# Performance work log

Hardware: AMD Instinct MI355X
Metric: run time of the kernel (lower is better)

Reference implementation:

```python
import jax, jax.numpy as jnp
import numpy as np

NEG_BIG = -9e15
ALPHA = 0.2  # leakyrelu slope


def setup_inputs() -> dict:
    key = jax.random.key(0)
    k1, k2, k3, k4 = jax.random.split(key, 4)
    N, Fin, Fout = 8192, 256, 256
    input = jax.random.normal(k1, (N, Fin), dtype=jnp.float32)
    adj = jax.random.randint(k2, (N, N), 0, 2, dtype=jnp.int32)
    W = jax.random.normal(k3, (Fin, Fout), dtype=jnp.float32) * (1.0 / np.sqrt(Fin))
    a = jax.random.normal(k4, (2 * Fout, 1), dtype=jnp.float32) * (1.0 / np.sqrt(Fout))
    return {"input": input, "adj": adj, "W": W, "a": a}


def reference(input, adj, W, a):
    # h: [N, F]
    h = input @ W
    Fout = h.shape[1]
    # Fused score: e_ij = leakyrelu(h_i . a[:F] + h_j . a[F:])
    s1 = h @ a[:Fout, 0]   # [N]
    s2 = h @ a[Fout:, 0]   # [N]
    e = s1[:, None] + s2[None, :]            # [N, N]
    e = jnp.where(e >= 0, e, ALPHA * e)      # leaky relu
    e = jnp.where(adj > 0, e, NEG_BIG)       # mask
    attention = jax.nn.softmax(e, axis=1)    # row softmax
    h_prime = attention @ h                  # [N, F]
    return jax.nn.elu(h_prime)               # concat=True -> elu
```

## Files before the change

kernel.cpp:

```cpp
#include <hip/hip_runtime.h>
#include <hip/hip_bf16.h>

#define LRALPHA 0.2f
#define LOG2E 1.4426950408889634f

typedef __attribute__((ext_vector_type(8))) short frag_ab;
typedef __attribute__((ext_vector_type(4))) float frag_cd;
typedef int   iv4 __attribute__((ext_vector_type(4)));
typedef float fv4 __attribute__((ext_vector_type(4)));
typedef unsigned int uv4 __attribute__((ext_vector_type(4)));
typedef unsigned int uv2 __attribute__((ext_vector_type(2)));

static __device__ __forceinline__ unsigned short f2bf(float f) {
  __hip_bfloat16 b = __float2bfloat16(f);
  unsigned short u;
  __builtin_memcpy(&u, &b, 2);
  return u;
}

#if __has_builtin(__builtin_amdgcn_exp2f)
#define EXP2F(x) __builtin_amdgcn_exp2f(x)
#else
#define EXP2F(x) exp2f(x)
#endif

static __device__ __forceinline__ unsigned cvt_pk_bf16(float lo, float hi) {
  unsigned r;
  asm("v_cvt_pk_bf16_f32 %0, %1, %2" : "=v"(r) : "v"(lo), "v"(hi));
  return r;
}

static __device__ __forceinline__ void block_sync_lds() {
  __builtin_amdgcn_sched_barrier(0);
  asm volatile("s_waitcnt lgkmcnt(0)" ::: "memory");
  __builtin_amdgcn_s_barrier();
  __builtin_amdgcn_sched_barrier(0);
}

static __device__ __forceinline__ uv2 make_w4(iv4 ca, fv4 cv,
                                              float s1r, float mr, float& zloc) {
  float w[4];
#pragma unroll
  for (int e = 0; e < 4; ++e) {
    float ee = s1r + cv[e];
    ee = fmaxf(ee, LRALPHA * ee);
    float ww = EXP2F(ee - mr);
    ww = ca[e] ? ww : 0.f;
    zloc += ww;
    w[e] = ww;
  }
  uv2 r;
  r[0] = cvt_pk_bf16(w[0], w[1]);
  r[1] = cvt_pk_bf16(w[2], w[3]);
  return r;
}

__global__ __launch_bounds__(256, 4) void gat_hproj(
    const float* __restrict__ X, const float* __restrict__ W,
    const float* __restrict__ avec,
    float* __restrict__ s1, float* __restrict__ s2,
    unsigned short* __restrict__ hT) {
  const int tid = threadIdx.x;
  const int row0 = blockIdx.x * 16;
  const float* Xb = X + (size_t)row0 * 256;
  const int c = tid;

  float acc[16];
#pragma unroll
  for (int r = 0; r < 16; ++r) acc[r] = 0.f;

  for (int k = 0; k < 256; k += 4) {
    const float w0 = W[(k + 0) * 256 + c];
    const float w1 = W[(k + 1) * 256 + c];
    const float w2 = W[(k + 2) * 256 + c];
    const float w3 = W[(k + 3) * 256 + c];
#pragma unroll
    for (int r = 0; r < 16; ++r) {
      acc[r] = fmaf(Xb[r * 256 + k + 0], w0, acc[r]);
      acc[r] = fmaf(Xb[r * 256 + k + 1], w1, acc[r]);
      acc[r] = fmaf(Xb[r * 256 + k + 2], w2, acc[r]);
      acc[r] = fmaf(Xb[r * 256 + k + 3], w3, acc[r]);
    }
  }

  alignas(16) unsigned short hu[16];
#pragma unroll
  for (int r = 0; r < 16; ++r) hu[r] = f2bf(acc[r]);
  uv4* hdst = (uv4*)(hT + (size_t)c * 8192 + row0);
  hdst[0] = *(const uv4*)&hu[0];
  hdst[1] = *(const uv4*)&hu[8];

  const float a1c = avec[c];
  const float a2c = avec[256 + c];
  const int lane = tid & 63, wave = tid >> 6;
  __shared__ float r1[4][16], r2[4][16];
#pragma unroll
  for (int r = 0; r < 16; ++r) {
    float v1 = acc[r] * a1c;
    float v2 = acc[r] * a2c;
#pragma unroll
    for (int off = 32; off > 0; off >>= 1) {
      v1 += __shfl_down(v1, off);
      v2 += __shfl_down(v2, off);
    }
    if (lane == 0) { r1[wave][r] = v1; r2[wave][r] = v2; }
  }
  __syncthreads();
  if (tid < 16) {
    s1[row0 + tid] = (r1[0][tid] + r1[1][tid] + r1[2][tid] + r1[3][tid]) * LOG2E;
    s2[row0 + tid] = (r2[0][tid] + r2[1][tid] + r2[2][tid] + r2[3][tid]) * LOG2E;
  }
}

__global__ __launch_bounds__(512, 2) void gat_attn_full(
    const int* __restrict__ adj, const unsigned short* __restrict__ hT,
    const float* __restrict__ s1, const float* __restrict__ s2,
    float* __restrict__ out) {
  const int bid = blockIdx.x;
  const int row0 = bid * 32;
  const int tid = threadIdx.x;
  const int wave = tid >> 6, lane = tid & 63;
  const int ln16 = lane & 15, quad = lane >> 4;

  __shared__ __align__(16) unsigned short P[2][32][72];
  __shared__ float Zred[32][16];
  __shared__ float wred[8];
  __shared__ float Zinv[32];

  float m = -1e30f;
  for (int i = tid; i < 8192; i += 512) m = fmaxf(m, s2[i]);
#pragma unroll
  for (int off = 32; off > 0; off >>= 1) m = fmaxf(m, __shfl_down(m, off));
  if (lane == 0) wred[wave] = m;
  __syncthreads();
  float s2m = wred[0];
#pragma unroll
  for (int wv = 1; wv < 8; ++wv) s2m = fmaxf(s2m, wred[wv]);

  const int r = tid >> 4;
  const int cg = tid & 15;
  const float s1r = s1[row0 + r];
  const float tmv = s1r + s2m;
  const float mr = tmv >= 0.f ? tmv : LRALPHA * tmv;

  const int* adjRow = adj + (size_t)(row0 + r) * 8192 + cg * 4;
  const float* s2p = s2 + cg * 4;

  frag_cd acc[2][2];
  const frag_cd fz = {0.f, 0.f, 0.f, 0.f};
#pragma unroll
  for (int mi = 0; mi < 2; ++mi)
#pragma unroll
    for (int ni = 0; ni < 2; ++ni) acc[mi][ni] = fz;

  float zloc = 0.f;
  const int NIT = 128;

  {
    iv4 ca = __builtin_nontemporal_load((const iv4*)adjRow);
    fv4 cv = *(const fv4*)s2p;
    *(uv2*)&P[0][r][cg * 4] = make_w4(ca, cv, s1r, mr, zloc);
  }
  iv4 a = __builtin_nontemporal_load((const iv4*)(adjRow + 64));
  fv4 v = *(const fv4*)(s2p + 64);
  block_sync_lds();

  for (int jt = 0; jt < NIT; ++jt) {
    const int cur = jt & 1, nxt = cur ^ 1;
    const size_t jbase = (size_t)jt * 64;

    frag_ab bf[2][2];
#pragma unroll
    for (int kk = 0; kk < 2; ++kk)
#pragma unroll
      for (int ni = 0; ni < 2; ++ni) {
        const int f = wave * 32 + ni * 16 + ln16;
        bf[kk][ni] = *(const frag_ab*)(hT + (size_t)f * 8192 + jbase + kk * 32 + quad * 8);
      }

    iv4 a2; fv4 v2;
    if (jt + 2 < NIT) {
      const int o = (jt + 2) * 64;
      a2 = __builtin_nontemporal_load((const iv4*)(adjRow + o));
      v2 = *(const fv4*)(s2p + o);
    }

    if (jt + 1 < NIT) {
      *(uv2*)&P[nxt][r][cg * 4] = make_w4(a, v, s1r, mr, zloc);
    }

#pragma unroll
    for (int kk = 0; kk < 2; ++kk) {
      frag_ab af[2];
#pragma unroll
      for (int mi = 0; mi < 2; ++mi)
        af[mi] = *(const frag_ab*)&P[cur][mi * 16 + ln16][kk * 32 + quad * 8];
#pragma unroll
      for (int mi = 0; mi < 2; ++mi)
#pragma unroll
        for (int ni = 0; ni < 2; ++ni)
          acc[mi][ni] = __builtin_amdgcn_mfma_f32_16x16x32_bf16(
              af[mi], bf[kk][ni], acc[mi][ni], 0, 0, 0);
    }
    block_sync_lds();
    a = a2; v = v2;
  }

  Zred[r][cg] = zloc;
  __syncthreads();
  if (tid < 32) {
    float z = 0.f;
#pragma unroll
    for (int q = 0; q < 16; ++q) z += Zred[tid][q];
    Zinv[tid] = 1.f / z;
  }
  __syncthreads();

  float* outb = out + (size_t)row0 * 256;
#pragma unroll
  for (int mi = 0; mi < 2; ++mi) {
#pragma unroll
    for (int ni = 0; ni < 2; ++ni) {
      const int f = wave * 32 + ni * 16 + ln16;
#pragma unroll
      for (int reg = 0; reg < 4; ++reg) {
        const int grow = mi * 16 + quad * 4 + reg;
        const float vv = acc[mi][ni][reg] * Zinv[grow];
        const float o = vv > 0.f ? vv : expm1f(vv);
        __builtin_nontemporal_store(o, outb + (size_t)grow * 256 + f);
      }
    }
  }
}

extern "C" void kernel_launch(void* const* d_in, const int* in_sizes, int n_in,
                              void* d_out, int out_size, void* d_ws, size_t ws_size,
                              hipStream_t stream) {
  const float* X = (const float*)d_in[0];
  const int* adj = (const int*)d_in[1];
  const float* W = (const float*)d_in[2];
  const float* avec = (const float*)d_in[3];
  float* out = (float*)d_out;

  float* wsf = (float*)d_ws;
  float* s1 = wsf;
  float* s2 = wsf + 8192;
  unsigned short* hT = (unsigned short*)(wsf + 16384);

  hipLaunchKernelGGL(gat_hproj, dim3(512), dim3(256), 0, stream, X, W, avec, s1, s2, hT);
  hipLaunchKernelGGL(gat_attn_full, dim3(256), dim3(512), 0, stream, adj, hT, s1, s2, out);
}
```

Baseline: 557.7 us.

## Double attention block size to 1024 threads and prefetch hT fragments

The attention kernel now runs 16 waves per block instead of 8. Each wave owns 16 output features rather than 32, and each thread builds 2 attention weights per tile instead of 4. The hT B-fragments are now loaded one iteration ahead in registers, so the global loads overlap the current tile's MFMAs. The aim is more latency hiding on the adjacency stream and the hT loads, at the cost of a larger block-wide barrier, narrower 8-byte adj loads, and duplicated P fragment reads across more waves.

```diff
diff --git a/kernel.cpp b/kernel.cpp
--- a/kernel.cpp
+++ b/kernel.cpp
@@ -8,8 +8,9 @@
 typedef __attribute__((ext_vector_type(4))) float frag_cd;
 typedef int   iv4 __attribute__((ext_vector_type(4)));
 typedef float fv4 __attribute__((ext_vector_type(4)));
+typedef int   iv2 __attribute__((ext_vector_type(2)));
+typedef float fv2 __attribute__((ext_vector_type(2)));
 typedef unsigned int uv4 __attribute__((ext_vector_type(4)));
-typedef unsigned int uv2 __attribute__((ext_vector_type(2)));
 
 static __device__ __forceinline__ unsigned short f2bf(float f) {
   __hip_bfloat16 b = __float2bfloat16(f);
@@ -37,11 +38,11 @@
   __builtin_amdgcn_sched_barrier(0);
 }
 
-static __device__ __forceinline__ uv2 make_w4(iv4 ca, fv4 cv,
-                                              float s1r, float mr, float& zloc) {
-  float w[4];
-#pragma unroll
-  for (int e = 0; e < 4; ++e) {
+static __device__ __forceinline__ unsigned make_w2(iv2 ca, fv2 cv,
+                                                   float s1r, float mr, float& zloc) {
+  float w[2];
+#pragma unroll
+  for (int e = 0; e < 2; ++e) {
     float ee = s1r + cv[e];
     ee = fmaxf(ee, LRALPHA * ee);
     float ww = EXP2F(ee - mr);
@@ -49,10 +50,7 @@
     zloc += ww;
     w[e] = ww;
   }
-  uv2 r;
-  r[0] = cvt_pk_bf16(w[0], w[1]);
-  r[1] = cvt_pk_bf16(w[2], w[3]);
-  return r;
+  return cvt_pk_bf16(w[0], w[1]);
 }
 
 __global__ __launch_bounds__(256, 4) void gat_hproj(
@@ -112,7 +110,7 @@
   }
 }
 
-__global__ __launch_bounds__(512, 2) void gat_attn_full(
+__global__ __launch_bounds__(1024, 4) void gat_attn_full(
     const int* __restrict__ adj, const unsigned short* __restrict__ hT,
     const float* __restrict__ s1, const float* __restrict__ s2,
     float* __restrict__ out) {
@@ -123,86 +121,81 @@
   const int ln16 = lane & 15, quad = lane >> 4;
 
   __shared__ __align__(16) unsigned short P[2][32][72];
-  __shared__ float Zred[32][16];
-  __shared__ float wred[8];
+  __shared__ float Zred[32][32];
+  __shared__ float wred[16];
   __shared__ float Zinv[32];
 
   float m = -1e30f;
-  for (int i = tid; i < 8192; i += 512) m = fmaxf(m, s2[i]);
+  for (int i = tid; i < 8192; i += 1024) m = fmaxf(m, s2[i]);
 #pragma unroll
   for (int off = 32; off > 0; off >>= 1) m = fmaxf(m, __shfl_down(m, off));
   if (lane == 0) wred[wave] = m;
   __syncthreads();
   float s2m = wred[0];
 #pragma unroll
-  for (int wv = 1; wv < 8; ++wv) s2m = fmaxf(s2m, wred[wv]);
-
-  const int r = tid >> 4;
-  const int cg = tid & 15;
+  for (int wv = 1; wv < 16; ++wv) s2m = fmaxf(s2m, wred[wv]);
+
+  const int r = tid >> 5;
+  const int cg = tid & 31;
   const float s1r = s1[row0 + r];
   const float tmv = s1r + s2m;
   const float mr = tmv >= 0.f ? tmv : LRALPHA * tmv;
 
-  const int* adjRow = adj + (size_t)(row0 + r) * 8192 + cg * 4;
-  const float* s2p = s2 + cg * 4;
-
-  frag_cd acc[2][2];
+  const int* adjRow = adj + (size_t)(row0 + r) * 8192 + cg * 2;
+  const float* s2p = s2 + cg * 2;
+  const unsigned short* hTw = hT + (size_t)(wave * 16 + ln16) * 8192 + quad * 8;
+
+  frag_cd acc[2];
   const frag_cd fz = {0.f, 0.f, 0.f, 0.f};
-#pragma unroll
-  for (int mi = 0; mi < 2; ++mi)
-#pragma unroll
-    for (int ni = 0; ni < 2; ++ni) acc[mi][ni] = fz;
+  acc[0] = fz; acc[1] = fz;
 
   float zloc = 0.f;
   const int NIT = 128;
 
   {
-    iv4 ca = __builtin_nontemporal_load((const iv4*)adjRow);
-    fv4 cv = *(const fv4*)s2p;
-    *(uv2*)&P[0][r][cg * 4] = make_w4(ca, cv, s1r, mr, zloc);
-  }
-  iv4 a = __builtin_nontemporal_load((const iv4*)(adjRow + 64));
-  fv4 v = *(const fv4*)(s2p + 64);
+    iv2 ca = __builtin_nontemporal_load((const iv2*)adjRow);
+    fv2 cv = *(const fv2*)s2p;
+    *(unsigned*)&P[0][r][cg * 2] = make_w2(ca, cv, s1r, mr, zloc);
+  }
+  iv2 a = __builtin_nontemporal_load((const iv2*)(adjRow + 64));
+  fv2 v = *(const fv2*)(s2p + 64);
+  frag_ab bfC0 = *(const frag_ab*)(hTw + 0);
+  frag_ab bfC1 = *(const frag_ab*)(hTw + 32);
   block_sync_lds();
 
   for (int jt = 0; jt < NIT; ++jt) {
     const int cur = jt & 1, nxt = cur ^ 1;
-    const size_t jbase = (size_t)jt * 64;
-
-    frag_ab bf[2][2];
-#pragma unroll
-    for (int kk = 0; kk < 2; ++kk)
-#pragma unroll
-      for (int ni = 0; ni < 2; ++ni) {
-        const int f = wave * 32 + ni * 16 + ln16;
-        bf[kk][ni] = *(const frag_ab*)(hT + (size_t)f * 8192 + jbase + kk * 32 + quad * 8);
-      }
-
-    iv4 a2; fv4 v2;
+
+    frag_ab bfN0, bfN1;
+    if (jt + 1 < NIT) {
+      const size_t jn = (size_t)(jt + 1) * 64;
+      bfN0 = *(const frag_ab*)(hTw + jn);
+      bfN1 = *(const frag_ab*)(hTw + jn + 32);
+    }
+
+    iv2 a2; fv2 v2;
     if (jt + 2 < NIT) {
       const int o = (jt + 2) * 64;
-      a2 = __builtin_nontemporal_load((const iv4*)(adjRow + o));
-      v2 = *(const fv4*)(s2p + o);
+      a2 = __builtin_nontemporal_load((const iv2*)(adjRow + o));
+      v2 = *(const fv2*)(s2p + o);
     }
 
     if (jt + 1 < NIT) {
-      *(uv2*)&P[nxt][r][cg * 4] = make_w4(a, v, s1r, mr, zloc);
-    }
-
-#pragma unroll
-    for (int kk = 0; kk < 2; ++kk) {
-      frag_ab af[2];
-#pragma unroll
-      for (int mi = 0; mi < 2; ++mi)
-        af[mi] = *(const frag_ab*)&P[cur][mi * 16 + ln16][kk * 32 + quad * 8];
-#pragma unroll
-      for (int mi = 0; mi < 2; ++mi)
-#pragma unroll
-        for (int ni = 0; ni < 2; ++ni)
-          acc[mi][ni] = __builtin_amdgcn_mfma_f32_16x16x32_bf16(
-              af[mi], bf[kk][ni], acc[mi][ni], 0, 0, 0);
+      *(unsigned*)&P[nxt][r][cg * 2] = make_w2(a, v, s1r, mr, zloc);
+    }
+
+    {
+      frag_ab af0 = *(const frag_ab*)&P[cur][ln16][quad * 8];
+      frag_ab af1 = *(const frag_ab*)&P[cur][16 + ln16][quad * 8];
+      acc[0] = __builtin_amdgcn_mfma_f32_16x16x32_bf16(af0, bfC0, acc[0], 0, 0, 0);
+      acc[1] = __builtin_amdgcn_mfma_f32_16x16x32_bf16(af1, bfC0, acc[1], 0, 0, 0);
+      frag_ab af2 = *(const frag_ab*)&P[cur][ln16][32 + quad * 8];
+      frag_ab af3 = *(const frag_ab*)&P[cur][16 + ln16][32 + quad * 8];
+      acc[0] = __builtin_amdgcn_mfma_f32_16x16x32_bf16(af2, bfC1, acc[0], 0, 0, 0);
+      acc[1] = __builtin_amdgcn_mfma_f32_16x16x32_bf16(af3, bfC1, acc[1], 0, 0, 0);
     }
     block_sync_lds();
+    bfC0 = bfN0; bfC1 = bfN1;
     a = a2; v = v2;
   }
 
@@ -211,24 +204,21 @@
   if (tid < 32) {
     float z = 0.f;
 #pragma unroll
-    for (int q = 0; q < 16; ++q) z += Zred[tid][q];
+    for (int q = 0; q < 32; ++q) z += Zred[tid][q];
     Zinv[tid] = 1.f / z;
   }
   __syncthreads();
 
   float* outb = out + (size_t)row0 * 256;
+  const int f = wave * 16 + ln16;
 #pragma unroll
   for (int mi = 0; mi < 2; ++mi) {
 #pragma unroll
-    for (int ni = 0; ni < 2; ++ni) {
-      const int f = wave * 32 + ni * 16 + ln16;
-#pragma unroll
-      for (int reg = 0; reg < 4; ++reg) {
-        const int grow = mi * 16 + quad * 4 + reg;
-        const float vv = acc[mi][ni][reg] * Zinv[grow];
-        const float o = vv > 0.f ? vv : expm1f(vv);
-        __builtin_nontemporal_store(o, outb + (size_t)grow * 256 + f);
-      }
+    for (int reg = 0; reg < 4; ++reg) {
+      const int grow = mi * 16 + quad * 4 + reg;
+      const float vv = acc[mi][reg] * Zinv[grow];
+      const float o = vv > 0.f ? vv : expm1f(vv);
+      __builtin_nontemporal_store(o, outb + (size_t)grow * 256 + f);
     }
   }
 }
@@ -248,5 +238,5 @@
   unsigned short* hT = (unsigned short*)(wsf + 16384);
 
   hipLaunchKernelGGL(gat_hproj, dim3(512), dim3(256), 0, stream, X, W, avec, s1, s2, hT);
-  hipLaunchKernelGGL(gat_attn_full, dim3(256), dim3(512), 0, stream, adj, hT, s1, s2, out);
-}
+  hipLaunchKernelGGL(gat_attn_full, dim3(256), dim3(1024), 0, stream, adj, hT, s1, s2, out);
+}
```

Measured after the change: 520.4 us. -6.7%, faster.
